# Kernel tuning notes

Measured on AMD Instinct MI355X. Metric: run time of the kernel, lower is better.

## Reference

```python
import jax, jax.numpy as jnp
import numpy as np

BS, N, H = 8, 2048, 512
NEG_INF = -1.0e9
LEAKY_SLOPE = 0.01  # torch nn.LeakyReLU default


def setup_inputs() -> dict:
    key = jax.random.key(0)
    ks = jax.random.split(key, 8)
    feats = jax.random.normal(ks[0], (BS, N, H), dtype=jnp.float32)
    # random 0/1 adjacency with self-loops so every row has >=1 neighbor
    adj = jax.random.randint(ks[1], (BS, N, N), 0, 2).astype(jnp.float32)
    adj = jnp.maximum(adj, jnp.eye(N, dtype=jnp.float32)[None])
    s = 1.0 / np.sqrt(H)
    return {
        "feats": feats,
        "adj_mat": adj,
        "fc_w": jax.random.normal(ks[2], (H, H), dtype=jnp.float32) * s,
        "fc_b": jax.random.normal(ks[3], (H,), dtype=jnp.float32) * s,
        "q_w": jax.random.normal(ks[4], (1, H), dtype=jnp.float32) * s,
        "q_b": jax.random.normal(ks[5], (1,), dtype=jnp.float32) * s,
        "k_w": jax.random.normal(ks[6], (1, H), dtype=jnp.float32) * s,
        "k_b": jax.random.normal(ks[7], (1,), dtype=jnp.float32) * s,
    }


def reference(feats, adj_mat, fc_w, fc_b, q_w, q_b, k_w, k_b):
    # feats: [bs, N, H]; torch Linear: x @ W.T + b
    feat_proj = jnp.einsum("bnh,oh->bno", feats, fc_w) + fc_b          # [bs, N, H]
    q = jnp.einsum("bnh,oh->bno", feat_proj, q_w) + q_b                # [bs, N, 1]
    k = jnp.einsum("bnh,oh->bno", feat_proj, k_w) + k_b                # [bs, N, 1]
    logits = q + jnp.swapaxes(k, 2, 1)                                 # [bs, N, N] broadcast add
    masked = logits + (1.0 - adj_mat) * NEG_INF
    masked = jnp.where(masked >= 0, masked, LEAKY_SLOPE * masked)      # LeakyReLU
    atten = jax.nn.softmax(masked, axis=-1)
    # dropout is identity in eval mode
    out = jnp.einsum("bnm,bmh->bnh", atten, feat_proj)
    return out + feats  # residual=True
```

## Files before the change

### kernel.cpp

```cpp
#include <hip/hip_runtime.h>
#include <hip/hip_bf16.h>
#include <cstdint>
#include <cstddef>

#define BSZ 8
#define NN 2048
#define HH 512
#define MROWS (BSZ * NN)
#define LOG2E 1.44269504088896f

typedef __attribute__((ext_vector_type(4))) float f32x4;
typedef __attribute__((ext_vector_type(8))) short short8;
typedef __attribute__((ext_vector_type(4))) unsigned short us4;
typedef __attribute__((ext_vector_type(4))) uint32_t u32x4;

#if __has_builtin(__builtin_amdgcn_exp2f)
#define EXP2(x) __builtin_amdgcn_exp2f(x)
#else
#define EXP2(x) __expf((x) * 0.69314718056f)
#endif

static __device__ __forceinline__ unsigned short f2bf(float f) {
    uint32_t u = __builtin_bit_cast(uint32_t, f);
    u += 0x7fffu + ((u >> 16) & 1u);
    return (unsigned short)(u >> 16);
}

static __device__ __forceinline__ void async16(const unsigned short* g, unsigned short* l) {
    __builtin_amdgcn_global_load_lds(
        (const __attribute__((address_space(1))) void*)g,
        (__attribute__((address_space(3))) void*)l, 16, 0, 0);
}

__global__ __launch_bounds__(256) void prep_kernel(
    const float* __restrict__ feats, const float* __restrict__ fc_w,
    unsigned short* __restrict__ feats_bf, unsigned short* __restrict__ fcw_bf) {
    const int bid = blockIdx.x;
    const int tid = threadIdx.x;
    if (bid < 2048) {
        const int base = bid * 1024 + tid;
#pragma unroll
        for (int j = 0; j < 4; ++j) {
            const int i = base + j * 256;
            f32x4 v = ((const f32x4*)feats)[i];
            us4 o;
#pragma unroll
            for (int c = 0; c < 4; ++c) o[c] = f2bf(v[c]);
            ((us4*)feats_bf)[i] = o;
        }
    } else {
        const int base = (bid - 2048) * 1024 + tid;
#pragma unroll
        for (int j = 0; j < 4; ++j) {
            const int i = base + j * 256;
            f32x4 v = ((const f32x4*)fc_w)[i];
            us4 o;
#pragma unroll
            for (int c = 0; c < 4; ++c) o[c] = f2bf(v[c]);
            ((us4*)fcw_bf)[i] = o;
        }
    }
}

__global__ __launch_bounds__(256) void k2_kernel(
    const unsigned short* __restrict__ A, const unsigned short* __restrict__ Bt,
    const float* __restrict__ fc_b, const float* __restrict__ q_w,
    const float* __restrict__ k_w, const float* __restrict__ adj,
    unsigned short* __restrict__ fpT, unsigned char* __restrict__ maskb,
    float* __restrict__ qpart, float* __restrict__ kpart) {
    const int bid = blockIdx.x;
    const int tid = threadIdx.x;
    if (bid < 512) {
        __shared__ alignas(16) unsigned short As[128 * 32];
        __shared__ alignas(16) unsigned short Bs[128 * 32];
        __shared__ float qred[2][128], kred[2][128];
        const int wave = tid >> 6, lane = tid & 63;
        const int wi = wave >> 1, wj = wave & 1;
        const int n0 = (bid & 3) * 128;
        const int i0 = (bid >> 2) * 128;
        const int K = HH;
        const int lrow = lane >> 2;
        const int lseg = (lane & 3) * 8;
        const int fro = (lane & 15) * 32 + (lane >> 4) * 8;
        f32x4 acc[4][4];
#pragma unroll
        for (int a = 0; a < 4; ++a)
#pragma unroll
            for (int c = 0; c < 4; ++c) acc[a][c] = (f32x4)(0.f);

        for (int k0 = 0; k0 < K; k0 += 32) {
            __syncthreads();
            {
                const int c0 = wave * 2;
                const unsigned short* ga = A + (size_t)(i0 + c0 * 16 + lrow) * K + k0 + lseg;
                async16(ga, &As[(c0 * 16) * 32]);
                async16(ga + (size_t)16 * K, &As[(c0 * 16 + 16) * 32]);
                const unsigned short* gb = Bt + (size_t)(n0 + c0 * 16 + lrow) * K + k0 + lseg;
                async16(gb, &Bs[(c0 * 16) * 32]);
                async16(gb + (size_t)16 * K, &Bs[(c0 * 16 + 16) * 32]);
            }
            __syncthreads();
            short8 af[4], bf[4];
#pragma unroll
            for (int t = 0; t < 4; ++t) af[t] = *(const short8*)&As[(wi * 64 + t * 16) * 32 + fro];
#pragma unroll
            for (int t = 0; t < 4; ++t) bf[t] = *(const short8*)&Bs[(wj * 64 + t * 16) * 32 + fro];
#pragma unroll
            for (int it = 0; it < 4; ++it)
#pragma unroll
                for (int jt = 0; jt < 4; ++jt)
                    acc[it][jt] = __builtin_amdgcn_mfma_f32_16x16x32_bf16(af[it], bf[jt], acc[it][jt], 0, 0, 0);
        }

        int colv[4]; float cbv[4], qwv[4], kwv[4];
#pragma unroll
        for (int jt = 0; jt < 4; ++jt) {
            colv[jt] = n0 + wj * 64 + jt * 16 + (lane & 15);
            cbv[jt] = fc_b[colv[jt]];
            qwv[jt] = q_w[colv[jt]];
            kwv[jt] = k_w[colv[jt]];
        }
        const int b = i0 >> 11;
        const int il = i0 & 2047;
#pragma unroll
        for (int jt = 0; jt < 4; ++jt) {
#pragma unroll
            for (int it = 0; it < 4; ++it) {
                const int rb = wi * 64 + it * 16 + ((lane >> 4) << 2);
                us4 o;
#pragma unroll
                for (int r = 0; r < 4; ++r) o[r] = f2bf(acc[it][jt][r] + cbv[jt]);
                *(us4*)(fpT + ((size_t)b * HH + colv[jt]) * NN + il + rb) = o;
            }
        }
#pragma unroll
        for (int it = 0; it < 4; ++it) {
#pragma unroll
            for (int r = 0; r < 4; ++r) {
                float pq = 0.f, pk = 0.f;
#pragma unroll
                for (int jt = 0; jt < 4; ++jt) {
                    float v = acc[it][jt][r] + cbv[jt];
                    pq += v * qwv[jt];
                    pk += v * kwv[jt];
                }
                for (int off = 1; off < 16; off <<= 1) {
                    pq += __shfl_xor(pq, off, 64);
                    pk += __shfl_xor(pk, off, 64);
                }
                if ((lane & 15) == 0) {
                    const int rr = wi * 64 + it * 16 + ((lane >> 4) << 2) + r;
                    qred[wj][rr] = pq;
                    kred[wj][rr] = pk;
                }
            }
        }
        __syncthreads();
        if (tid < 128) {
            const size_t o = (size_t)(n0 >> 7) * MROWS + i0 + tid;
            qpart[o] = qred[0][tid] + qred[1][tid];
            kpart[o] = kred[0][tid] + kred[1][tid];
        }
    } else {
        const int a = bid - 512;
        const int wave = tid >> 6, lane = tid & 63;
#pragma unroll
        for (int s = 0; s < 2; ++s) {
            const int row = a * 8 + s * 4 + wave;
            const float* ar = adj + (size_t)row * NN;
#pragma unroll
            for (int p = 0; p < 4; ++p) {
                f32x4 v0 = *(const f32x4*)&ar[p * 512 + lane * 8];
                f32x4 v1 = *(const f32x4*)&ar[p * 512 + lane * 8 + 4];
                float fb = v0[0] + 2.f * v0[1] + 4.f * v0[2] + 8.f * v0[3]
                         + 16.f * v1[0] + 32.f * v1[1] + 64.f * v1[2] + 128.f * v1[3];
                maskb[(size_t)row * 256 + p * 64 + lane] = (unsigned char)(unsigned int)fb;
            }
        }
    }
}

__global__ __launch_bounds__(256) void fused_pv_kernel(
    const unsigned short* __restrict__ fpT, const unsigned char* __restrict__ maskb,
    const float* __restrict__ qpart, const float* __restrict__ kpart,
    const float* __restrict__ q_b, const float* __restrict__ k_b,
    const float* __restrict__ feats, float* __restrict__ out) {
    __shared__ alignas(16) unsigned short As[64 * 32];
    __shared__ alignas(16) unsigned short Bs[256 * 32];
    __shared__ float kLDS[NN];
    __shared__ float qLDS[64];
    __shared__ float zfl[256];
    __shared__ float rzl[64];
    const int tid = threadIdx.x;
    const int wave = tid >> 6, lane = tid & 63;
    const int wi = wave >> 1, wj = wave & 1;
    const int bid = blockIdx.x;
    const int b = bid & 7;
    const int t6 = bid >> 3;
    const int i0 = (t6 >> 1) * 64;
    const int n0 = (t6 & 1) * 256;
    const size_t rowbase = (size_t)b * NN + i0;

    {
        const float kb = k_b[0], qb = q_b[0];
#pragma unroll
        for (int s = 0; s < 8; ++s) {
            const int j = s * 256 + tid;
            const size_t gj = (size_t)b * NN + j;
            kLDS[j] = (kpart[gj] + kpart[MROWS + gj] + kpart[2 * MROWS + gj]
                     + kpart[3 * MROWS + gj] + kb) * LOG2E;
        }
        if (tid < 64) {
            const size_t gi = rowbase + tid;
            qLDS[tid] = (qpart[gi] + qpart[MROWS + gi] + qpart[2 * MROWS + gi]
                       + qpart[3 * MROWS + gi] + qb) * LOG2E;
        }
    }
    __syncthreads();

    const int r0 = tid >> 2;
    const int c8 = (tid & 3) * 8;
    const float qi = qLDS[r0];
    float z = 0.f;

    const unsigned short* Bt = fpT + (size_t)b * HH * NN;
    const uint32_t* mk = (const uint32_t*)maskb;
    const size_t mrow = (rowbase + r0) * 64;
    const int lrow = lane >> 2, lseg = (lane & 3) * 8;
    const int fro = (lane & 15) * 32 + (lane >> 4) * 8;

    f32x4 acc[2][8];
#pragma unroll
    for (int a = 0; a < 2; ++a)
#pragma unroll
        for (int c = 0; c < 8; ++c) acc[a][c] = (f32x4)(0.f);

    uint32_t mcur = mk[mrow];
    for (int k0 = 0; k0 < NN; k0 += 32) {
        __syncthreads();
        {
            const int rbase = wave * 64;
            const unsigned short* gb = Bt + (size_t)(n0 + rbase + lrow) * NN + k0 + lseg;
            async16(gb, &Bs[rbase * 32]);
            async16(gb + (size_t)16 * NN, &Bs[(rbase + 16) * 32]);
            async16(gb + (size_t)32 * NN, &Bs[(rbase + 32) * 32]);
            async16(gb + (size_t)48 * NN, &Bs[(rbase + 48) * 32]);
        }
        uint32_t mnext = 0;
        if (k0 + 32 < NN) mnext = mk[mrow + ((k0 + 32) >> 5)];
        const f32x4 kv0 = *(const f32x4*)&kLDS[k0 + c8];
        const f32x4 kv1 = *(const f32x4*)&kLDS[k0 + c8 + 4];
        const uint32_t byte8 = (mcur >> c8) & 0xffu;
        float wv[8];
#pragma unroll
        for (int c = 0; c < 8; ++c) {
            float s = qi + (c < 4 ? kv0[c] : kv1[c - 4]);
            s = fmaxf(s, 0.01f * s);
            float e = EXP2(s);
            wv[c] = ((byte8 >> c) & 1u) ? e : 0.f;
            z += wv[c];
        }
        u32x4 pk;
#pragma unroll
        for (int p = 0; p < 4; ++p) {
            uint32_t lo = __builtin_bit_cast(uint32_t, wv[2 * p]) + 0x8000u;
            uint32_t hi = __builtin_bit_cast(uint32_t, wv[2 * p + 1]) + 0x8000u;
            pk[p] = __builtin_amdgcn_perm(hi, lo, 0x07060302u);
        }
        *(u32x4*)&As[r0 * 32 + c8] = pk;
        __syncthreads();
        short8 af[2], bf[8];
#pragma unroll
        for (int t = 0; t < 2; ++t) af[t] = *(const short8*)&As[(wi * 32 + t * 16) * 32 + fro];
#pragma unroll
        for (int t = 0; t < 8; ++t) bf[t] = *(const short8*)&Bs[(wj * 128 + t * 16) * 32 + fro];
#pragma unroll
        for (int it = 0; it < 2; ++it)
#pragma unroll
            for (int jt = 0; jt < 8; ++jt)
                acc[it][jt] = __builtin_amdgcn_mfma_f32_16x16x32_bf16(af[it], bf[jt], acc[it][jt], 0, 0, 0);
        mcur = mnext;
    }

    zfl[tid] = z;
    __syncthreads();
    if (tid < 64) {
        const float* zp = &zfl[tid * 4];
        rzl[tid] = 1.0f / (zp[0] + zp[1] + zp[2] + zp[3]);
    }
    __syncthreads();

#pragma unroll
    for (int it = 0; it < 2; ++it) {
        const int rb = wi * 32 + it * 16 + ((lane >> 4) << 2);
        float rv[4];
#pragma unroll
        for (int r = 0; r < 4; ++r) rv[r] = rzl[rb + r];
#pragma unroll
        for (int jt = 0; jt < 8; ++jt) {
            const int col = n0 + wj * 128 + jt * 16 + (lane & 15);
#pragma unroll
            for (int r = 0; r < 4; ++r) {
                const size_t idx = (rowbase + rb + r) * HH + col;
                out[idx] = acc[it][jt][r] * rv[r] + feats[idx];
            }
        }
    }
}

extern "C" void kernel_launch(void* const* d_in, const int* in_sizes, int n_in,
                              void* d_out, int out_size, void* d_ws, size_t ws_size,
                              hipStream_t stream) {
    const float* feats = (const float*)d_in[0];
    const float* adj   = (const float*)d_in[1];
    const float* fc_w  = (const float*)d_in[2];
    const float* fc_b  = (const float*)d_in[3];
    const float* q_w   = (const float*)d_in[4];
    const float* q_b   = (const float*)d_in[5];
    const float* k_w   = (const float*)d_in[6];
    const float* k_b   = (const float*)d_in[7];
    float* out = (float*)d_out;

    char* w = (char*)d_ws;
    auto alloc = [&](size_t bytes) {
        char* p = w;
        w += (bytes + 255) & ~(size_t)255;
        return p;
    };
    unsigned short* feats_bf = (unsigned short*)alloc((size_t)BSZ * NN * HH * 2);
    unsigned short* fcw_bf   = (unsigned short*)alloc((size_t)HH * HH * 2);
    unsigned short* fpT   = (unsigned short*)alloc((size_t)BSZ * HH * NN * 2);
    unsigned char*  maskb = (unsigned char*)alloc((size_t)MROWS * 256);
    float* qpart = (float*)alloc((size_t)4 * MROWS * 4);
    float* kpart = (float*)alloc((size_t)4 * MROWS * 4);

    prep_kernel<<<2112, 256, 0, stream>>>(feats, fc_w, feats_bf, fcw_bf);
    k2_kernel<<<512 + 2048, 256, 0, stream>>>(feats_bf, fcw_bf, fc_b, q_w, k_w, adj,
                                              fpT, maskb, qpart, kpart);
    fused_pv_kernel<<<512, 256, 0, stream>>>(
        fpT, maskb, qpart, kpart, q_b, k_b, feats, out);
}
```

Measured before the change: 323.9 us.

## Double-buffer LDS tiles and compute softmax denominator via MFMA with ones

```diff
diff --git a/kernel.cpp b/kernel.cpp
--- a/kernel.cpp
+++ b/kernel.cpp
@@ -185,11 +185,10 @@
     const float* __restrict__ qpart, const float* __restrict__ kpart,
     const float* __restrict__ q_b, const float* __restrict__ k_b,
     const float* __restrict__ feats, float* __restrict__ out) {
-    __shared__ alignas(16) unsigned short As[64 * 32];
-    __shared__ alignas(16) unsigned short Bs[256 * 32];
+    __shared__ alignas(16) unsigned short As[2][64 * 32];
+    __shared__ alignas(16) unsigned short Bs[2][256 * 32];
     __shared__ float kLDS[NN];
     __shared__ float qLDS[64];
-    __shared__ float zfl[256];
     __shared__ float rzl[64];
     const int tid = threadIdx.x;
     const int wave = tid >> 6, lane = tid & 63;
@@ -221,7 +220,6 @@
     const int r0 = tid >> 2;
     const int c8 = (tid & 3) * 8;
     const float qi = qLDS[r0];
-    float z = 0.f;
 
     const unsigned short* Bt = fpT + (size_t)b * HH * NN;
     const uint32_t* mk = (const uint32_t*)maskb;
@@ -229,64 +227,85 @@
     const int lrow = lane >> 2, lseg = (lane & 3) * 8;
     const int fro = (lane & 15) * 32 + (lane >> 4) * 8;
 
-    f32x4 acc[2][8];
-#pragma unroll
-    for (int a = 0; a < 2; ++a)
-#pragma unroll
-        for (int c = 0; c < 8; ++c) acc[a][c] = (f32x4)(0.f);
-
-    uint32_t mcur = mk[mrow];
-    for (int k0 = 0; k0 < NN; k0 += 32) {
-        __syncthreads();
-        {
-            const int rbase = wave * 64;
-            const unsigned short* gb = Bt + (size_t)(n0 + rbase + lrow) * NN + k0 + lseg;
-            async16(gb, &Bs[rbase * 32]);
-            async16(gb + (size_t)16 * NN, &Bs[(rbase + 16) * 32]);
-            async16(gb + (size_t)32 * NN, &Bs[(rbase + 32) * 32]);
-            async16(gb + (size_t)48 * NN, &Bs[(rbase + 48) * 32]);
-        }
-        uint32_t mnext = 0;
-        if (k0 + 32 < NN) mnext = mk[mrow + ((k0 + 32) >> 5)];
+    auto stageB = [&](int buf, int k0) {
+        const int rbase = wave * 64;
+        const unsigned short* gb = Bt + (size_t)(n0 + rbase + lrow) * NN + k0 + lseg;
+        async16(gb, &Bs[buf][rbase * 32]);
+        async16(gb + (size_t)16 * NN, &Bs[buf][(rbase + 16) * 32]);
+        async16(gb + (size_t)32 * NN, &Bs[buf][(rbase + 32) * 32]);
+        async16(gb + (size_t)48 * NN, &Bs[buf][(rbase + 48) * 32]);
+    };
+    auto transform = [&](int buf, int k0, uint32_t mbits) {
         const f32x4 kv0 = *(const f32x4*)&kLDS[k0 + c8];
         const f32x4 kv1 = *(const f32x4*)&kLDS[k0 + c8 + 4];
-        const uint32_t byte8 = (mcur >> c8) & 0xffu;
+        const uint32_t byte8 = (mbits >> c8) & 0xffu;
         float wv[8];
 #pragma unroll
         for (int c = 0; c < 8; ++c) {
             float s = qi + (c < 4 ? kv0[c] : kv1[c - 4]);
             s = fmaxf(s, 0.01f * s);
-            float e = EXP2(s);
+            const float e = EXP2(s);
             wv[c] = ((byte8 >> c) & 1u) ? e : 0.f;
-            z += wv[c];
         }
         u32x4 pk;
 #pragma unroll
         for (int p = 0; p < 4; ++p) {
-            uint32_t lo = __builtin_bit_cast(uint32_t, wv[2 * p]) + 0x8000u;
-            uint32_t hi = __builtin_bit_cast(uint32_t, wv[2 * p + 1]) + 0x8000u;
+            const uint32_t lo = __builtin_bit_cast(uint32_t, wv[2 * p]);
+            const uint32_t hi = __builtin_bit_cast(uint32_t, wv[2 * p + 1]);
             pk[p] = __builtin_amdgcn_perm(hi, lo, 0x07060302u);
         }
-        *(u32x4*)&As[r0 * 32 + c8] = pk;
-        __syncthreads();
+        *(u32x4*)&As[buf][r0 * 32 + c8] = pk;
+    };
+
+    f32x4 acc[2][8];
+#pragma unroll
+    for (int a = 0; a < 2; ++a)
+#pragma unroll
+        for (int c = 0; c < 8; ++c) acc[a][c] = (f32x4)(0.f);
+    f32x4 acc_z[2] = {(f32x4)(0.f), (f32x4)(0.f)};
+    short8 ones;
+#pragma unroll
+    for (int j = 0; j < 8; ++j) ones[j] = (short)0x3F80;
+
+    stageB(0, 0);
+    transform(0, 0, mk[mrow]);
+    uint32_t mnext = mk[mrow + 1];
+    __syncthreads();
+
+    for (int k0 = 0; k0 < NN; k0 += 32) {
+        const int p = (k0 >> 5) & 1;
+        if (k0 + 32 < NN) {
+            stageB(p ^ 1, k0 + 32);
+            uint32_t mfar = 0;
+            if (k0 + 64 < NN) mfar = mk[mrow + ((k0 + 64) >> 5)];
+            transform(p ^ 1, k0 + 32, mnext);
+            mnext = mfar;
+        }
         short8 af[2], bf[8];
 #pragma unroll
-        for (int t = 0; t < 2; ++t) af[t] = *(const short8*)&As[(wi * 32 + t * 16) * 32 + fro];
-#pragma unroll
-        for (int t = 0; t < 8; ++t) bf[t] = *(const short8*)&Bs[(wj * 128 + t * 16) * 32 + fro];
+        for (int t = 0; t < 2; ++t) af[t] = *(const short8*)&As[p][(wi * 32 + t * 16) * 32 + fro];
+#pragma unroll
+        for (int t = 0; t < 8; ++t) bf[t] = *(const short8*)&Bs[p][(wj * 128 + t * 16) * 32 + fro];
 #pragma unroll
         for (int it = 0; it < 2; ++it)
 #pragma unroll
             for (int jt = 0; jt < 8; ++jt)
                 acc[it][jt] = __builtin_amdgcn_mfma_f32_16x16x32_bf16(af[it], bf[jt], acc[it][jt], 0, 0, 0);
-        mcur = mnext;
-    }
-
-    zfl[tid] = z;
-    __syncthreads();
-    if (tid < 64) {
-        const float* zp = &zfl[tid * 4];
-        rzl[tid] = 1.0f / (zp[0] + zp[1] + zp[2] + zp[3]);
+        if (wj == 0) {
+#pragma unroll
+            for (int it = 0; it < 2; ++it)
+                acc_z[it] = __builtin_amdgcn_mfma_f32_16x16x32_bf16(af[it], ones, acc_z[it], 0, 0, 0);
+        }
+        __syncthreads();
+    }
+
+    if (wj == 0 && (lane & 15) == 0) {
+#pragma unroll
+        for (int it = 0; it < 2; ++it) {
+            const int rb = wi * 32 + it * 16 + ((lane >> 4) << 2);
+#pragma unroll
+            for (int r = 0; r < 4; ++r) rzl[rb + r] = 1.0f / acc_z[it][r];
+        }
     }
     __syncthreads();
 
```

After: 314.0 us. 1.03x faster.
